# Kernel tuning notes

Hardware: AMD Instinct MI355X
Metric: run time of the kernel (lower is better)

The kernel has to match this reference:

```python
import jax, jax.numpy as jnp
import numpy as np

R_EPS = 1e-15

def _sdf_net(x, W1, b1, W2, b2):
    h = jax.nn.relu(x @ W1 + b1)
    return h @ W2 + b2  # [..., 1+feat]

def _fd_gradient(x, W1, b1, W2, b2, eps):
    # central finite differences of the SDF along the 3 axes
    offs = eps * jnp.eye(3, dtype=x.dtype)              # [3,3]
    xp = x[None, :, :] + offs[:, None, :]               # [3,P,3]
    xm = x[None, :, :] - offs[:, None, :]
    sp = _sdf_net(xp, W1, b1, W2, b2)[..., 0]           # [3,P]
    sm = _sdf_net(xm, W1, b1, W2, b2)[..., 0]
    return ((sp - sm) / (2.0 * eps)).T                  # [P,3]

def _softplus100(x):
    # torch.nn.Softplus(beta=100)
    return jax.nn.softplus(100.0 * x) / 100.0

def _exclusive_cumprod(a):
    ones = jnp.ones_like(a[:, :1])
    return jnp.cumprod(jnp.concatenate([ones, a], -1), -1)[:, :-1]

def _sample_pdf(bins, weights, n_samples):
    # bins [R,K], weights [R,K-1]; deterministic inverse-CDF sampling (det=True)
    weights = weights + 1e-5
    pdf = weights / jnp.sum(weights, -1, keepdims=True)
    cdf = jnp.cumsum(pdf, -1)
    cdf = jnp.concatenate([jnp.zeros_like(cdf[:, :1]), cdf], -1)  # [R,K]
    K = cdf.shape[-1]
    u = jnp.linspace(0.5 / n_samples, 1.0 - 0.5 / n_samples, n_samples, dtype=bins.dtype)
    u = jnp.broadcast_to(u[None], (bins.shape[0], n_samples))
    inds = jax.vmap(lambda c, uu: jnp.searchsorted(c, uu, side='right'))(cdf, u)
    below = jnp.clip(inds - 1, 0, K - 1)
    above = jnp.clip(inds, 0, K - 1)
    cdf_b = jnp.take_along_axis(cdf, below, -1)
    cdf_a = jnp.take_along_axis(cdf, above, -1)
    bin_b = jnp.take_along_axis(bins, below, -1)
    bin_a = jnp.take_along_axis(bins, above, -1)
    denom = cdf_a - cdf_b
    denom = jnp.where(denom < 1e-5, jnp.ones_like(denom), denom)
    t = (u - cdf_b) / denom
    return bin_b + t * (bin_a - bin_b)

def _forward(rays_o, rays_d, W1, b1, W2, b2, Wc1, bc1, Wc2, bc2, inv_s_param,
             num_steps, upsample_steps, bound):
    B, N = rays_o.shape[:2]
    ro = rays_o.reshape(-1, 3)
    rd = rays_d.reshape(-1, 3)
    R = ro.shape[0]
    bnd = float(bound)
    # near/far from cube bound
    tmin = (-bnd - ro) / (rd + R_EPS)
    tmax = (bnd - ro) / (rd + R_EPS)
    near = jnp.max(jnp.minimum(tmin, tmax), -1, keepdims=True)
    far = jnp.min(jnp.maximum(tmin, tmax), -1, keepdims=True)
    near = jnp.maximum(near, 0.05)
    z = jnp.linspace(0.0, 1.0, num_steps, dtype=ro.dtype)[None]
    z_vals = near + (far - near) * z                     # [R,S0]
    sample_dist = (far - near) / num_steps               # [R,1]
    pts = ro[:, None, :] + rd[:, None, :] * z_vals[..., None]
    pts = jnp.clip(pts, -bnd, bnd)
    # --- coarse SDF pass + inverse-CDF importance resampling (torch.no_grad) ---
    sdf_c = _sdf_net(pts.reshape(-1, 3), W1, b1, W2, b2)[:, 0].reshape(R, num_steps)
    sdf_c = jax.lax.stop_gradient(sdf_c)
    d_c = z_vals[:, 1:] - z_vals[:, :-1]
    mid_sdf = 0.5 * (sdf_c[:, 1:] + sdf_c[:, :-1])
    cos_val = jnp.clip((sdf_c[:, 1:] - sdf_c[:, :-1]) / (d_c + 1e-5), -1e3, 0.0)
    prev_c = jax.nn.sigmoid((mid_sdf - cos_val * d_c * 0.5) * 64.0)
    next_c = jax.nn.sigmoid((mid_sdf + cos_val * d_c * 0.5) * 64.0)
    alpha_c = jnp.clip((prev_c - next_c + 1e-5) / (prev_c + 1e-5), 0.0, 1.0)
    w_c = alpha_c * _exclusive_cumprod(1.0 - alpha_c + 1e-7)
    new_z = jax.lax.stop_gradient(_sample_pdf(z_vals, w_c, upsample_steps))
    z_vals = jnp.sort(jnp.concatenate([z_vals, new_z], -1), -1)
    S = num_steps + upsample_steps
    # --- fine pass: deltas / midpoints / shading / NeuS compositing ---
    deltas = z_vals[:, 1:] - z_vals[:, :-1]
    deltas = jnp.concatenate([deltas, jnp.broadcast_to(sample_dist, (R, 1))], -1)
    z_mid = jnp.concatenate([z_vals[:, :-1] + 0.5 * deltas[:, :-1], z_vals[:, -1:]], -1)
    new_pts = ro[:, None, :] + rd[:, None, :] * z_mid[..., None]
    new_pts = jnp.clip(new_pts, -bnd, bnd)
    flat_pts = new_pts.reshape(-1, 3)                    # [R*S,3]
    out = _sdf_net(flat_pts, W1, b1, W2, b2)
    sdf = out[:, :1]
    feat = out[:, 1:]
    grad = _fd_gradient(flat_pts, W1, b1, W2, b2, 0.005)  # eps=0.005*(1-ratio), ratio=0
    normal = grad / (1e-5 + jnp.linalg.norm(grad, axis=-1, keepdims=True))
    dirs = jnp.broadcast_to(rd[:, None, :], new_pts.shape).reshape(-1, 3)
    cin = jnp.concatenate([flat_pts, dirs, normal, feat], -1)
    color = jax.nn.sigmoid(jax.nn.relu(cin @ Wc1 + bc1) @ Wc2 + bc2)   # [R*S,3]
    inv_s = jnp.exp(10.0 * inv_s_param)                   # forward_variance()
    true_cos = jnp.sum(dirs * normal, -1, keepdims=True)
    iter_cos = -_softplus100(-true_cos)                   # cos_anneal_ratio = 1.0
    d_flat = deltas.reshape(-1, 1)
    prev_cdf = jax.nn.sigmoid((sdf - iter_cos * d_flat * 0.5) * inv_s)
    next_cdf = jax.nn.sigmoid((sdf + iter_cos * d_flat * 0.5) * inv_s)
    alpha = jnp.clip((prev_cdf - next_cdf + 1e-5) / (prev_cdf + 1e-5), 0.0, 1.0).reshape(R, S)
    weights = alpha * _exclusive_cumprod(1.0 - alpha + 1e-7)
    weights_sum = jnp.sum(weights, -1, keepdims=True)
    image = jnp.sum(color.reshape(R, S, 3) * weights[..., None], 1)
    image = image + (1.0 - weights_sum) * 1.0             # bg_color = 1
    return image.reshape(B, N, 3)

def setup_inputs() -> dict:
    key = jax.random.key(0)
    ks = jax.random.split(key, 8)
    B, N, H, F = 1, 4096, 64, 64
    rays_o = (jax.random.uniform(ks[0], (B, N, 3), jnp.float32) - 0.5) * 0.5
    d = jax.random.normal(ks[1], (B, N, 3), jnp.float32)
    rays_d = d / (1e-8 + jnp.linalg.norm(d, axis=-1, keepdims=True))
    def lin(k, i, o):
        return jax.random.normal(k, (i, o), jnp.float32) / np.sqrt(i).astype(np.float32)
    W1 = lin(ks[2], 3, H); b1 = jnp.zeros((H,), jnp.float32)
    W2 = lin(ks[3], H, 1 + F); b2 = jnp.zeros((1 + F,), jnp.float32)
    Wc1 = lin(ks[4], 9 + F, H); bc1 = jnp.zeros((H,), jnp.float32)
    Wc2 = lin(ks[5], H, 3); bc2 = jnp.zeros((3,), jnp.float32)
    inv_s_param = jnp.full((1,), 0.3, jnp.float32)
    return {"rays_o": rays_o, "rays_d": rays_d, "W1": W1, "b1": b1, "W2": W2, "b2": b2,
            "Wc1": Wc1, "bc1": bc1, "Wc2": Wc2, "bc2": bc2, "inv_s_param": inv_s_param,
            "num_steps": 64, "upsample_steps": 64, "bound": 1}

def reference(rays_o, rays_d, W1, b1, W2, b2, Wc1, bc1, Wc2, bc2, inv_s_param,
              num_steps, upsample_steps, bound):
    return _forward(rays_o, rays_d, W1, b1, W2, b2, Wc1, bc1, Wc2, bc2, inv_s_param,
                    num_steps, upsample_steps, bound)
```

## Files before the change

kernel.cpp:

```cpp
#include <hip/hip_runtime.h>
#include <hip/hip_bf16.h>
#include <cmath>

#define KS 84

#define OFF_W1    0
#define OFF_W1E   256
#define OFF_W1S   512
#define OFF_WC2   768
#define OFF_BC2   1024
#define OFF_GC    1028
#define OFF_AF    1032

typedef __attribute__((ext_vector_type(4))) short  short4v;
typedef __attribute__((ext_vector_type(8))) short  short8v;
typedef __attribute__((ext_vector_type(16))) float f32x16;

__device__ __forceinline__ float sigm(float x){ return 1.0f/(1.0f + expf(-x)); }
__device__ __forceinline__ float clampf(float x, float lo, float hi){ return fminf(fmaxf(x, lo), hi); }
__device__ __forceinline__ unsigned short f2bf(float x){
  __hip_bfloat16 h = __float2bfloat16(x);
  return *reinterpret_cast<unsigned short*>(&h);
}
__device__ __forceinline__ unsigned cvt_pk_bf16(float a, float b){
  unsigned r;
  asm("v_cvt_pk_bf16_f32 %0, %1, %2" : "=v"(r) : "v"(a), "v"(b));
  return r;
}
__device__ __forceinline__ short8v lds_load8(const unsigned short* p){
  short4v lo = *(const short4v*)p;
  short4v hi = *(const short4v*)(p + 4);
  short8v r;
  r[0]=lo[0]; r[1]=lo[1]; r[2]=lo[2]; r[3]=lo[3];
  r[4]=hi[0]; r[5]=hi[1]; r[6]=hi[2]; r[7]=hi[3];
  return r;
}

__global__ __launch_bounds__(256)
void prep_weights(const float* __restrict__ W1, const float* __restrict__ b1,
                  const float* __restrict__ W2, const float* __restrict__ b2,
                  const float* __restrict__ Wc1, const float* __restrict__ bc1,
                  const float* __restrict__ Wc2, const float* __restrict__ bc2,
                  float* __restrict__ ws)
{
  __shared__ float LW2[4160];
  __shared__ float LWc1[4672];
  __shared__ float LW1[192];
  __shared__ float Lb1[64];
  __shared__ float Lb2[65];
  __shared__ float Lbc1[64];
  __shared__ float LWc2[192];
  __shared__ float Lbc2[3];
  __shared__ float s_cb[4][64];
  __shared__ unsigned short W2T[64*KS];
  __shared__ unsigned short ABUF[64*KS];
  const int tid  = threadIdx.x;
  const int lane = tid & 63;
  const int wv   = tid >> 6;
  const int l31  = lane & 31;
  const int h    = lane >> 5;

  {
    const float4* s4 = (const float4*)W2;
    float4* d4 = (float4*)LW2;
    for (int i = tid; i < 1040; i += 256) d4[i] = s4[i];
    const float4* c4 = (const float4*)Wc1;
    float4* e4 = (float4*)LWc1;
    for (int i = tid; i < 1168; i += 256) e4[i] = c4[i];
  }
  if (tid < 192) LW1[tid]  = W1[tid];
  if (tid < 64)  Lb1[tid]  = b1[tid];
  if (tid < 65)  Lb2[tid]  = b2[tid];
  if (tid < 64)  Lbc1[tid] = bc1[tid];
  if (tid < 192) LWc2[tid] = Wc2[tid];
  if (tid < 3)   Lbc2[tid] = bc2[tid];
  __syncthreads();

  for (int i = tid; i < 4096; i += 256){
    int k = i >> 6, t = i & 63;
    W2T[k*KS + t] = f2bf(LW2[k*65 + 1 + t]);
  }
  for (int i = tid; i < 576; i += 256){
    int ii = i >> 6, c = i & 63;
    ABUF[c*KS + 64 + ii] = f2bf(LWc1[ii*64 + c]);
  }
  for (int i = tid; i < 384; i += 256){
    int z = i >> 6, c = i & 63;
    ABUF[c*KS + 74 + z] = 0;
  }
  {
    int c = tid & 63, q = tid >> 6;
    float acc = 0.f;
    #pragma unroll
    for (int t = 16*q; t < 16*q + 16; ++t)
      acc = fmaf(Lb2[1+t], LWc1[(9+t)*64 + c], acc);
    s_cb[q][c] = acc;
  }
  if (tid < 64){
    int j = tid;
    float wx = LW1[j], wy = LW1[64+j], wz = LW1[128+j];
    float w2 = LW2[j*65];
    float Hx = 0.005f * fabsf(wx);
    float Hy = 0.005f * fabsf(wy);
    float Hz = 0.005f * fabsf(wz);
    float Sx = (wx < 0.f) ? -w2 : w2;
    float Sy = (wy < 0.f) ? -w2 : w2;
    float Sz = (wz < 0.f) ? -w2 : w2;
    ws[OFF_W1 + 4*j + 0] = wx;
    ws[OFF_W1 + 4*j + 1] = wy;
    ws[OFF_W1 + 4*j + 2] = wz;
    ws[OFF_W1 + 4*j + 3] = Lb1[j];
    ws[OFF_W1E + 4*j + 0] = Hx;
    ws[OFF_W1E + 4*j + 1] = Hy;
    ws[OFF_W1E + 4*j + 2] = Hz;
    ws[OFF_W1E + 4*j + 3] = w2;
    ws[OFF_W1S + 4*j + 0] = Sx;
    ws[OFF_W1S + 4*j + 1] = Sy;
    ws[OFF_W1S + 4*j + 2] = Sz;
    ws[OFF_W1S + 4*j + 3] = 0.f;
    float sx = Sx*Hx, sy = Sy*Hy, sz = Sz*Hz;
    #pragma unroll
    for (int off = 1; off < 64; off <<= 1){
      sx += __shfl_xor(sx, off);
      sy += __shfl_xor(sy, off);
      sz += __shfl_xor(sz, off);
    }
    if (j == 0){
      ws[OFF_GC + 0] = sx;
      ws[OFF_GC + 1] = sy;
      ws[OFF_GC + 2] = sz;
    }
  } else if (tid < 128){
    int j = tid - 64;
    ws[OFF_WC2 + 4*j + 0] = LWc2[j*3+0];
    ws[OFF_WC2 + 4*j + 1] = LWc2[j*3+1];
    ws[OFF_WC2 + 4*j + 2] = LWc2[j*3+2];
    ws[OFF_WC2 + 4*j + 3] = 0.f;
  } else if (tid < 132){
    int j = tid - 128;
    ws[OFF_BC2 + j] = (j < 3) ? Lbc2[j] : Lb2[0];
  }
  __syncthreads();

  if (tid < 64){
    float acc = Lbc1[tid] + ((s_cb[0][tid] + s_cb[1][tid]) + (s_cb[2][tid] + s_cb[3][tid]));
    ABUF[tid*KS + 73] = f2bf(acc);
  }
  {
    const int mb = wv & 1, kb = wv >> 1;
    f32x16 e;
    #pragma unroll
    for (int i = 0; i < 16; ++i) e[i] = 0.f;
    #pragma unroll
    for (int s = 0; s < 4; ++s){
      short8v afr;
      #pragma unroll
      for (int j = 0; j < 8; ++j)
        afr[j] = (short)f2bf(LWc1[(9 + 16*s + 8*h + j)*64 + 32*mb + l31]);
      short8v bfr = lds_load8(&W2T[(32*kb + l31)*KS + 16*s + 8*h]);
      e = __builtin_amdgcn_mfma_f32_32x32x16_bf16(afr, bfr, e, 0, 0, 0);
    }
    const int kcol = 32*kb + l31;
    #pragma unroll
    for (int r = 0; r < 16; ++r){
      int c = 32*mb + (r & 3) + 8*(r >> 2) + 4*h;
      ABUF[c*KS + kcol] = f2bf(e[r]);
    }
  }
  __syncthreads();

  for (int i = tid; i < 640; i += 256){
    int f = i >> 6, ln = i & 63;
    int mb = f / 5, kk = f - 5*mb;
    int c  = 32*mb + (ln & 31);
    int kb2 = 16*kk + 8*(ln >> 5);
    short8v v = lds_load8(&ABUF[c*KS + kb2]);
    *((short8v*)(((unsigned short*)(ws + OFF_AF)) + (size_t)i * 8)) = v;
  }
}

__global__ __launch_bounds__(64, 8)
void neus_render(const float* __restrict__ rays_o, const float* __restrict__ rays_d,
                 const float* __restrict__ inv_s_p, const float* __restrict__ ws,
                 float* __restrict__ out)
{
  __shared__ unsigned short s_aext[64*KS];
  __shared__ float4 s_wc2[64];
  __shared__ float  s_z[64];
  __shared__ float  s_cdf[64];
  __shared__ float  s_newz[64];
  __shared__ float  s_zall[128];

  const int lane = threadIdx.x;
  const int ray  = blockIdx.x;

  const float4* __restrict__ pW1  = (const float4*)(ws + OFF_W1);
  const float4* __restrict__ pW1E = (const float4*)(ws + OFF_W1E);
  const float4* __restrict__ pW1S = (const float4*)(ws + OFF_W1S);
  const float*  __restrict__ pbc2 = ws + OFF_BC2;
  const float*  __restrict__ pgc  = ws + OFF_GC;
  const float b20 = pbc2[3];

  s_wc2[lane] = ((const float4*)(ws + OFF_WC2))[lane];

  float ox = rays_o[ray*3], oy = rays_o[ray*3+1], oz = rays_o[ray*3+2];
  float dx = rays_d[ray*3], dy = rays_d[ray*3+1], dz = rays_d[ray*3+2];
  const float inv_s = expf(10.f * inv_s_p[0]);
  float tnx = (-1.f-ox)/(dx+1e-15f), tfx = (1.f-ox)/(dx+1e-15f);
  float tny = (-1.f-oy)/(dy+1e-15f), tfy = (1.f-oy)/(dy+1e-15f);
  float tnz = (-1.f-oz)/(dz+1e-15f), tfz = (1.f-oz)/(dz+1e-15f);
  float nearv = fmaxf(fmaxf(fminf(tnx,tfx), fminf(tny,tfy)), fminf(tnz,tfz));
  float farv  = fminf(fminf(fmaxf(tnx,tfx), fmaxf(tny,tfy)), fmaxf(tnz,tfz));
  nearv = fmaxf(nearv, 0.05f);
  const float sd = (farv - nearv) * (1.f/64.f);

  {
    float zt = nearv + (farv-nearv) * ((float)lane * (1.f/63.f));
    float px = clampf(ox + dx*zt, -1.f, 1.f);
    float py = clampf(oy + dy*zt, -1.f, 1.f);
    float pz = clampf(oz + dz*zt, -1.f, 1.f);
    float acc0 = b20, acc1 = 0.f;
    #pragma unroll 4
    for (int q = 0; q < 32; ++q){
      int j = 2*q;
      float4 wa = pW1[j];
      float4 wb = pW1[j+1];
      float ea = pW1E[j].w;
      float eb = pW1E[j+1].w;
      float ha = fmaxf(fmaf(px, wa.x, fmaf(py, wa.y, fmaf(pz, wa.z, wa.w))), 0.f);
      float hb = fmaxf(fmaf(px, wb.x, fmaf(py, wb.y, fmaf(pz, wb.z, wb.w))), 0.f);
      acc0 = fmaf(ha, ea, acc0);
      acc1 = fmaf(hb, eb, acc1);
    }
    float acc = acc0 + acc1;
    s_z[lane] = zt;
    float s1  = __shfl_down(acc, 1);
    float zt1 = nearv + (farv-nearv) * ((float)(lane+1) * (1.f/63.f));
    float a_c = 0.f, qv = 1.f;
    if (lane < 63){
      float dc   = zt1 - zt;
      float mid  = 0.5f*(acc + s1);
      float cosv = clampf((s1-acc)/(dc+1e-5f), -1000.f, 0.f);
      float est  = cosv*dc*0.5f;
      float pcv  = sigm((mid-est)*64.f);
      float ncv  = sigm((mid+est)*64.f);
      a_c = clampf((pcv-ncv+1e-5f)/(pcv+1e-5f), 0.f, 1.f);
      qv  = 1.f - a_c + 1e-7f;
    }
    float p = qv;
    #pragma unroll
    for (int off = 1; off < 64; off <<= 1){
      float t = __shfl_up(p, off);
      if (lane >= off) p *= t;
    }
    float ec = __shfl_up(p, 1);
    if (lane == 0) ec = 1.f;
    float wvv = (lane < 63) ? (a_c*ec + 1e-5f) : 0.f;
    float tot = wvv;
    #pragma unroll
    for (int off = 32; off > 0; off >>= 1) tot += __shfl_xor(tot, off);
    float cs = wvv;
    #pragma unroll
    for (int off = 1; off < 64; off <<= 1){
      float t = __shfl_up(cs, off);
      if (lane >= off) cs += t;
    }
    if (lane == 0)  s_cdf[0] = 0.f;
    if (lane < 63)  s_cdf[lane+1] = cs / tot;
  }
  __syncthreads();

  {
    float u = ((float)lane + 0.5f) * (1.f/64.f);
    int lo = 0, hi = 64;
    while (lo < hi){
      int m = (lo+hi) >> 1;
      if (s_cdf[m] <= u) lo = m+1; else hi = m;
    }
    int below = lo - 1;
    int above = lo < 63 ? lo : 63;
    float cb = s_cdf[below], ca = s_cdf[above];
    float bb = s_z[below],   ba = s_z[above];
    float den = ca - cb; if (den < 1e-5f) den = 1.f;
    float tt = (u - cb)/den;
    s_newz[lane] = bb + tt*(ba - bb);
  }
  __syncthreads();

  const short8v* pAF = (const short8v*)(ws + OFF_AF);
  short8v af[10];
  #pragma unroll
  for (int f = 0; f < 10; ++f) af[f] = pAF[f*64 + lane];

  {
    float v0 = s_z[lane];
    int lo0 = 0, hi0 = 64;
    while (lo0 < hi0){ int m=(lo0+hi0)>>1; if (s_newz[m] < v0) lo0 = m+1; else hi0 = m; }
    float v1 = s_newz[lane];
    int lo1 = 0, hi1 = 64;
    while (lo1 < hi1){ int m=(lo1+hi1)>>1; if (s_z[m] <= v1) lo1 = m+1; else hi1 = m; }
    s_zall[lane + lo0] = v0;
    s_zall[lane + lo1] = v1;
  }
  __syncthreads();

  unsigned short* arow = &s_aext[(unsigned)lane * KS];
  const unsigned short* aw = s_aext;
  const int scol = lane & 31;
  const int half8 = (lane >> 5) * 8;
  const int halfoff = (lane >> 5) * 4;
  const bool hihalf = (lane >= 32);
  const float gc0 = pgc[0], gc1 = pgc[1], gc2 = pgc[2];
  float rA = 0.f, rB = 0.f, rC = 0.f, rD = 0.f;
  float Tc = 1.f;

  for (int b = 0; b < 2; ++b){
    const int lt2 = 64*b + lane;
    float zc = s_zall[lt2];
    float zn = s_zall[lt2 < 127 ? lt2+1 : 127];
    float delta = (lt2 < 127) ? (zn - zc) : sd;
    float zm    = (lt2 < 127) ? (zc + 0.5f*delta) : zc;
    float px = clampf(ox + dx*zm, -1.f, 1.f);
    float py = clampf(oy + dy*zm, -1.f, 1.f);
    float pz = clampf(oz + dz*zm, -1.f, 1.f);

    float sa0 = b20, sa1 = 0.f;
    float gxa = gc0, gya = gc1, gza = gc2;
    float gxb = 0.f, gyb = 0.f, gzb = 0.f;
    #pragma unroll 2
    for (int q = 0; q < 16; ++q){
      int j = 4*q;
      float4 w0 = pW1[j],   e0 = pW1E[j],   s0 = pW1S[j];
      float4 w1 = pW1[j+1], e1 = pW1E[j+1], s1v = pW1S[j+1];
      float4 w2 = pW1[j+2], e2 = pW1E[j+2], s2v = pW1S[j+2];
      float4 w3 = pW1[j+3], e3 = pW1E[j+3], s3v = pW1S[j+3];
      float base0 = fmaf(px, w0.x, fmaf(py, w0.y, fmaf(pz, w0.z, w0.w)));
      float base1 = fmaf(px, w1.x, fmaf(py, w1.y, fmaf(pz, w1.z, w1.w)));
      float base2 = fmaf(px, w2.x, fmaf(py, w2.y, fmaf(pz, w2.z, w2.w)));
      float base3 = fmaf(px, w3.x, fmaf(py, w3.y, fmaf(pz, w3.z, w3.w)));
      float hv0 = fmaxf(base0, 0.f), hv1 = fmaxf(base1, 0.f);
      float hv2 = fmaxf(base2, 0.f), hv3 = fmaxf(base3, 0.f);
      sa0 = fmaf(hv0, e0.w, sa0); sa0 = fmaf(hv1, e1.w, sa0);
      sa1 = fmaf(hv2, e2.w, sa1); sa1 = fmaf(hv3, e3.w, sa1);
      gxa = fmaf(__builtin_amdgcn_fmed3f(base0, -e0.x, e0.x), s0.x, gxa);
      gya = fmaf(__builtin_amdgcn_fmed3f(base0, -e0.y, e0.y), s0.y, gya);
      gza = fmaf(__builtin_amdgcn_fmed3f(base0, -e0.z, e0.z), s0.z, gza);
      gxa = fmaf(__builtin_amdgcn_fmed3f(base1, -e1.x, e1.x), s1v.x, gxa);
      gya = fmaf(__builtin_amdgcn_fmed3f(base1, -e1.y, e1.y), s1v.y, gya);
      gza = fmaf(__builtin_amdgcn_fmed3f(base1, -e1.z, e1.z), s1v.z, gza);
      gxb = fmaf(__builtin_amdgcn_fmed3f(base2, -e2.x, e2.x), s2v.x, gxb);
      gyb = fmaf(__builtin_amdgcn_fmed3f(base2, -e2.y, e2.y), s2v.y, gyb);
      gzb = fmaf(__builtin_amdgcn_fmed3f(base2, -e2.z, e2.z), s2v.z, gzb);
      gxb = fmaf(__builtin_amdgcn_fmed3f(base3, -e3.x, e3.x), s3v.x, gxb);
      gyb = fmaf(__builtin_amdgcn_fmed3f(base3, -e3.y, e3.y), s3v.y, gyb);
      gzb = fmaf(__builtin_amdgcn_fmed3f(base3, -e3.z, e3.z), s3v.z, gzb);
      *(unsigned*)&arow[j]   = cvt_pk_bf16(hv0, hv1);
      *(unsigned*)&arow[j+2] = cvt_pk_bf16(hv2, hv3);
    }
    float sdfv = sa0 + sa1;
    float gx = (gxa+gxb)*100.f, gy = (gya+gyb)*100.f, gz = (gza+gzb)*100.f;
    float gn = 1e-5f + sqrtf(gx*gx + gy*gy + gz*gz);
    float nx = gx/gn, ny = gy/gn, nz = gz/gn;

    *(unsigned*)&arow[64] = cvt_pk_bf16(px, py);
    *(unsigned*)&arow[66] = cvt_pk_bf16(pz, dx);
    *(unsigned*)&arow[68] = cvt_pk_bf16(dy, dz);
    *(unsigned*)&arow[70] = cvt_pk_bf16(nx, ny);
    *(unsigned*)&arow[72] = cvt_pk_bf16(nz, 1.0f);
    *(unsigned*)&arow[74] = 0u;
    *(unsigned*)&arow[76] = 0u;
    *(unsigned*)&arow[78] = 0u;

    float tcos = dx*nx + dy*ny + dz*nz;
    float aarg = -100.f * tcos;
    float spv  = (aarg > 0.f) ? (aarg + log1pf(expf(-aarg))) : log1pf(expf(aarg));
    float iter_cos = -(spv * 0.01f);
    float est = iter_cos * delta * 0.5f;
    float pcv = sigm((sdfv - est)*inv_s);
    float ncv = sigm((sdfv + est)*inv_s);
    float alpha = clampf((pcv - ncv + 1e-5f)/(pcv + 1e-5f), 0.f, 1.f);

    float qv = 1.f - alpha + 1e-7f;
    float p = qv;
    #pragma unroll
    for (int off = 1; off < 64; off <<= 1){
      float t = __shfl_up(p, off);
      if (lane >= off) p *= t;
    }
    float excl = __shfl_up(p, 1);
    if (lane == 0) excl = 1.f;
    excl *= Tc;
    float w = alpha * excl;
    Tc *= __shfl(p, 63);

    __syncthreads();

    f32x16 acc00, acc01, acc10, acc11;
    #pragma unroll
    for (int i = 0; i < 16; ++i){ acc00[i]=0.f; acc01[i]=0.f; acc10[i]=0.f; acc11[i]=0.f; }
    #pragma unroll
    for (int kk = 0; kk < 5; ++kk){
      int koff = 16*kk + half8;
      short8v b0 = lds_load8(&aw[ scol      * KS + koff]);
      short8v b1 = lds_load8(&aw[(32+scol) * KS + koff]);
      acc00 = __builtin_amdgcn_mfma_f32_32x32x16_bf16(af[kk],   b0, acc00, 0, 0, 0);
      acc10 = __builtin_amdgcn_mfma_f32_32x32x16_bf16(af[5+kk], b0, acc10, 0, 0, 0);
      acc01 = __builtin_amdgcn_mfma_f32_32x32x16_bf16(af[kk],   b1, acc01, 0, 0, 0);
      acc11 = __builtin_amdgcn_mfma_f32_32x32x16_bf16(af[5+kk], b1, acc11, 0, 0, 0);
    }

    float pr0=0.f,pr1=0.f,pr2=0.f,pr3=0.f,pr4=0.f,pr5=0.f;
    #pragma unroll
    for (int r = 0; r < 16; ++r){
      int ci = (r & 3) + 8*(r >> 2) + halfoff;
      float4 wA = s_wc2[ci];
      float4 wB = s_wc2[32 + ci];
      float v;
      v = fmaxf(acc00[r], 0.f); pr0 = fmaf(v, wA.x, pr0); pr1 = fmaf(v, wA.y, pr1); pr2 = fmaf(v, wA.z, pr2);
      v = fmaxf(acc10[r], 0.f); pr0 = fmaf(v, wB.x, pr0); pr1 = fmaf(v, wB.y, pr1); pr2 = fmaf(v, wB.z, pr2);
      v = fmaxf(acc01[r], 0.f); pr3 = fmaf(v, wA.x, pr3); pr4 = fmaf(v, wA.y, pr4); pr5 = fmaf(v, wA.z, pr5);
      v = fmaxf(acc11[r], 0.f); pr3 = fmaf(v, wB.x, pr3); pr4 = fmaf(v, wB.y, pr4); pr5 = fmaf(v, wB.z, pr5);
    }
    pr0 += __shfl_xor(pr0, 32); pr1 += __shfl_xor(pr1, 32); pr2 += __shfl_xor(pr2, 32);
    pr3 += __shfl_xor(pr3, 32); pr4 += __shfl_xor(pr4, 32); pr5 += __shfl_xor(pr5, 32);
    float c0 = sigm((hihalf ? pr3 : pr0) + pbc2[0]);
    float c1 = sigm((hihalf ? pr4 : pr1) + pbc2[1]);
    float c2 = sigm((hihalf ? pr5 : pr2) + pbc2[2]);

    rA += w; rB += w*c0; rC += w*c1; rD += w*c2;

    __syncthreads();
  }

  #pragma unroll
  for (int off = 32; off > 0; off >>= 1){
    rA += __shfl_xor(rA, off);
    rB += __shfl_xor(rB, off);
    rC += __shfl_xor(rC, off);
    rD += __shfl_xor(rD, off);
  }
  if (lane == 0){
    float bg = 1.f - rA;
    out[ray*3+0] = rB + bg;
    out[ray*3+1] = rC + bg;
    out[ray*3+2] = rD + bg;
  }
}

extern "C" void kernel_launch(void* const* d_in, const int* in_sizes, int n_in,
                              void* d_out, int out_size, void* d_ws, size_t ws_size,
                              hipStream_t stream)
{
  const float* rays_o = (const float*)d_in[0];
  const float* rays_d = (const float*)d_in[1];
  const float* W1  = (const float*)d_in[2];
  const float* b1  = (const float*)d_in[3];
  const float* W2  = (const float*)d_in[4];
  const float* b2  = (const float*)d_in[5];
  const float* Wc1 = (const float*)d_in[6];
  const float* bc1 = (const float*)d_in[7];
  const float* Wc2 = (const float*)d_in[8];
  const float* bc2 = (const float*)d_in[9];
  const float* inv_s = (const float*)d_in[10];
  float* out = (float*)d_out;
  float* ws  = (float*)d_ws;

  prep_weights<<<1, 256, 0, stream>>>(W1, b1, W2, b2, Wc1, bc1, Wc2, bc2, ws);

  const int R = in_sizes[0] / 3;
  dim3 grid(R), block(64);
  neus_render<<<grid, block, 0, stream>>>(rays_o, rays_d, inv_s, ws, out);
}
```

Before: 123.5 us.

## Pack two rays per block and replace block barriers with wave-local fences

Each 128-thread block now processes two rays, one per wavefront, with per-wave copies of all shared buffers. The __syncthreads calls become a wave-local fence: an lgkmcnt wait plus a scheduling barrier, relying on each wave touching only its own LDS slice. This halves the block count and drops cross-wave barrier cost. Risks: the s_wc2 fill is still indexed by the local lane (both waves write the same 64 entries) and is no longer followed by a block barrier, the launch-bounds occupancy hint is removed, and an odd ray count would drop the last ray.

New measurement: 126.3 us. 2.3% more time.

```diff
diff --git a/kernel.cpp b/kernel.cpp
--- a/kernel.cpp
+++ b/kernel.cpp
@@ -34,6 +34,10 @@
   r[0]=lo[0]; r[1]=lo[1]; r[2]=lo[2]; r[3]=lo[3];
   r[4]=hi[0]; r[5]=hi[1]; r[6]=hi[2]; r[7]=hi[3];
   return r;
+}
+__device__ __forceinline__ void wave_fence(){
+  asm volatile("s_waitcnt lgkmcnt(0)" ::: "memory");
+  __builtin_amdgcn_sched_barrier(0);
 }
 
 __global__ __launch_bounds__(256)
@@ -179,20 +183,21 @@
   }
 }
 
-__global__ __launch_bounds__(64, 8)
+__global__ __launch_bounds__(128)
 void neus_render(const float* __restrict__ rays_o, const float* __restrict__ rays_d,
                  const float* __restrict__ inv_s_p, const float* __restrict__ ws,
                  float* __restrict__ out)
 {
-  __shared__ unsigned short s_aext[64*KS];
+  __shared__ unsigned short s_aext[2][64*KS];
   __shared__ float4 s_wc2[64];
-  __shared__ float  s_z[64];
-  __shared__ float  s_cdf[64];
-  __shared__ float  s_newz[64];
-  __shared__ float  s_zall[128];
-
-  const int lane = threadIdx.x;
-  const int ray  = blockIdx.x;
+  __shared__ float  s_z[2][64];
+  __shared__ float  s_cdf[2][64];
+  __shared__ float  s_newz[2][64];
+  __shared__ float  s_zall[2][128];
+
+  const int lane = threadIdx.x & 63;
+  const int wir  = threadIdx.x >> 6;
+  const int ray  = blockIdx.x * 2 + wir;
 
   const float4* __restrict__ pW1  = (const float4*)(ws + OFF_W1);
   const float4* __restrict__ pW1E = (const float4*)(ws + OFF_W1E);
@@ -233,7 +238,7 @@
       acc1 = fmaf(hb, eb, acc1);
     }
     float acc = acc0 + acc1;
-    s_z[lane] = zt;
+    s_z[wir][lane] = zt;
     float s1  = __shfl_down(acc, 1);
     float zt1 = nearv + (farv-nearv) * ((float)(lane+1) * (1.f/63.f));
     float a_c = 0.f, qv = 1.f;
@@ -265,27 +270,27 @@
       float t = __shfl_up(cs, off);
       if (lane >= off) cs += t;
     }
-    if (lane == 0)  s_cdf[0] = 0.f;
-    if (lane < 63)  s_cdf[lane+1] = cs / tot;
-  }
-  __syncthreads();
+    if (lane == 0)  s_cdf[wir][0] = 0.f;
+    if (lane < 63)  s_cdf[wir][lane+1] = cs / tot;
+  }
+  wave_fence();
 
   {
     float u = ((float)lane + 0.5f) * (1.f/64.f);
     int lo = 0, hi = 64;
     while (lo < hi){
       int m = (lo+hi) >> 1;
-      if (s_cdf[m] <= u) lo = m+1; else hi = m;
+      if (s_cdf[wir][m] <= u) lo = m+1; else hi = m;
     }
     int below = lo - 1;
     int above = lo < 63 ? lo : 63;
-    float cb = s_cdf[below], ca = s_cdf[above];
-    float bb = s_z[below],   ba = s_z[above];
+    float cb = s_cdf[wir][below], ca = s_cdf[wir][above];
+    float bb = s_z[wir][below],   ba = s_z[wir][above];
     float den = ca - cb; if (den < 1e-5f) den = 1.f;
     float tt = (u - cb)/den;
-    s_newz[lane] = bb + tt*(ba - bb);
-  }
-  __syncthreads();
+    s_newz[wir][lane] = bb + tt*(ba - bb);
+  }
+  wave_fence();
 
   const short8v* pAF = (const short8v*)(ws + OFF_AF);
   short8v af[10];
@@ -293,19 +298,19 @@
   for (int f = 0; f < 10; ++f) af[f] = pAF[f*64 + lane];
 
   {
-    float v0 = s_z[lane];
+    float v0 = s_z[wir][lane];
     int lo0 = 0, hi0 = 64;
-    while (lo0 < hi0){ int m=(lo0+hi0)>>1; if (s_newz[m] < v0) lo0 = m+1; else hi0 = m; }
-    float v1 = s_newz[lane];
+    while (lo0 < hi0){ int m=(lo0+hi0)>>1; if (s_newz[wir][m] < v0) lo0 = m+1; else hi0 = m; }
+    float v1 = s_newz[wir][lane];
     int lo1 = 0, hi1 = 64;
-    while (lo1 < hi1){ int m=(lo1+hi1)>>1; if (s_z[m] <= v1) lo1 = m+1; else hi1 = m; }
-    s_zall[lane + lo0] = v0;
-    s_zall[lane + lo1] = v1;
-  }
-  __syncthreads();
-
-  unsigned short* arow = &s_aext[(unsigned)lane * KS];
-  const unsigned short* aw = s_aext;
+    while (lo1 < hi1){ int m=(lo1+hi1)>>1; if (s_z[wir][m] <= v1) lo1 = m+1; else hi1 = m; }
+    s_zall[wir][lane + lo0] = v0;
+    s_zall[wir][lane + lo1] = v1;
+  }
+  wave_fence();
+
+  unsigned short* arow = &s_aext[wir][(unsigned)lane * KS];
+  const unsigned short* aw = s_aext[wir];
   const int scol = lane & 31;
   const int half8 = (lane >> 5) * 8;
   const int halfoff = (lane >> 5) * 4;
@@ -316,8 +321,8 @@
 
   for (int b = 0; b < 2; ++b){
     const int lt2 = 64*b + lane;
-    float zc = s_zall[lt2];
-    float zn = s_zall[lt2 < 127 ? lt2+1 : 127];
+    float zc = s_zall[wir][lt2];
+    float zn = s_zall[wir][lt2 < 127 ? lt2+1 : 127];
     float delta = (lt2 < 127) ? (zn - zc) : sd;
     float zm    = (lt2 < 127) ? (zc + 0.5f*delta) : zc;
     float px = clampf(ox + dx*zm, -1.f, 1.f);
@@ -393,7 +398,7 @@
     float w = alpha * excl;
     Tc *= __shfl(p, 63);
 
-    __syncthreads();
+    wave_fence();
 
     f32x16 acc00, acc01, acc10, acc11;
     #pragma unroll
@@ -429,7 +434,7 @@
 
     rA += w; rB += w*c0; rC += w*c1; rD += w*c2;
 
-    __syncthreads();
+    wave_fence();
   }
 
   #pragma unroll
@@ -468,6 +473,6 @@
   prep_weights<<<1, 256, 0, stream>>>(W1, b1, W2, b2, Wc1, bc1, Wc2, bc2, ws);
 
   const int R = in_sizes[0] / 3;
-  dim3 grid(R), block(64);
+  dim3 grid(R / 2), block(128);
   neus_render<<<grid, block, 0, stream>>>(rays_o, rays_d, inv_s, ws, out);
 }
```
